# Performance work log

Hardware: AMD Instinct MI355X
Metric: run time of the kernel (lower is better)

## Reference

```python
import jax, jax.numpy as jnp
import numpy as np

N_NODES = 100000
N_EDGES = 1000000
D_IN = 256
D_OUT = 64


def setup_inputs() -> dict:
    key = jax.random.key(0)
    k1, k2, k3, k4, k5, k6 = jax.random.split(key, 6)
    x = jax.random.normal(k1, (N_NODES, D_IN), dtype=jnp.float32)
    # Xavier-style uniform init: stdv = 1/sqrt(output_dim)
    stdv = 1.0 / np.sqrt(D_OUT)
    weight = jax.random.uniform(k2, (D_IN, D_OUT), dtype=jnp.float32, minval=-stdv, maxval=stdv)
    adj_vals = jax.random.uniform(k3, (N_EDGES,), dtype=jnp.float32)
    prelu_a = jnp.full((1,), 0.25, dtype=jnp.float32)  # nn.PReLU default
    row = jax.random.randint(k4, (N_EDGES,), 0, N_NODES, dtype=jnp.int32)
    col = jax.random.randint(k5, (N_EDGES,), 0, N_NODES, dtype=jnp.int32)
    return {"x": x, "weight": weight, "adj_vals": adj_vals, "prelu_a": prelu_a,
            "row": row, "col": col}


def reference(x, weight, adj_vals, prelu_a, row, col):
    # dense GEMM: [N, D_in] @ [D_in, D_out]
    hidden = x @ weight  # gc_drop=0 -> identity dropout
    # sparse adj spmm: out[i] = sum_{e: row[e]=i} adj_vals[e] * hidden[col[e]]
    msg = adj_vals[:, None] * hidden[col]  # [E, D_out]
    agg = jax.ops.segment_sum(msg, row, num_segments=N_NODES)  # [N, D_out]
    # PReLU with single shared slope
    out = jnp.where(agg > 0, agg, prelu_a * agg)
    return out
```

## Files before the change

kernel.cpp:

```cpp
#include <hip/hip_runtime.h>

#define N_NODES 100000
#define N_EDGES 1000000
#define D_IN    256
#define D_OUT   64

#define BKT_SHIFT   4
#define NODES_PER_BKT 16
#define N_BKT       6250
#define BKT_CAP     256
#define EPB         2048
#define BIN_BLOCKS  489
#define GEMM_BLOCKS 782
#define NUM_TILES   6250
#define AGG_BLOCKS  782

typedef __attribute__((ext_vector_type(8))) short short8;
typedef __attribute__((ext_vector_type(4))) float f32x4;
typedef __attribute__((ext_vector_type(4))) unsigned short u16x4;

__device__ __forceinline__ unsigned short f2bf(float f) {
    unsigned int u = __float_as_uint(f);
    u = (u + 0x7fffu + ((u >> 16) & 1u)) >> 16;
    return (unsigned short)u;
}

__device__ __forceinline__ void mfma_store_tile(
    const short8 afrag[8], const unsigned short wT[64][272],
    unsigned short* __restrict__ hiddenBf, int r0, int n16, int quad)
{
    f32x4 acc[4] = {{0.f,0.f,0.f,0.f},{0.f,0.f,0.f,0.f},
                    {0.f,0.f,0.f,0.f},{0.f,0.f,0.f,0.f}};
#pragma unroll
    for (int ct = 0; ct < 4; ++ct) {
#pragma unroll
        for (int kk = 0; kk < 8; ++kk) {
            short8 b = *(const short8*)&wT[ct * 16 + n16][kk * 32 + quad * 8];
            acc[ct] = __builtin_amdgcn_mfma_f32_16x16x32_bf16(
                afrag[kk], b, acc[ct], 0, 0, 0);
        }
    }
#pragma unroll
    for (int ct = 0; ct < 4; ++ct)
#pragma unroll
        for (int reg = 0; reg < 4; ++reg)
            hiddenBf[(size_t)(r0 + quad * 4 + reg) * D_OUT + ct * 16 + n16]
                = f2bf(acc[ct][reg]);
}

__global__ __launch_bounds__(256, 2) void gemm_kernel(
    const float* __restrict__ x, const float* __restrict__ w,
    unsigned short* __restrict__ hiddenBf, int* __restrict__ gCursor)
{
    const int t = threadIdx.x;

    if (blockIdx.x == 0) {
        for (int i = t; i < N_BKT; i += 256) gCursor[i] = 0;
    }

    __shared__ unsigned short wT[64][272];

    for (int i = 0; i < 64; ++i) {
        int idx = t + i * 256;
        int k = idx >> 6, n = idx & 63;
        wT[n][k] = f2bf(w[idx]);
    }
    __syncthreads();

    const int lane = t & 63;
    const int wid  = t >> 6;
    const int n16  = lane & 15;
    const int quad = lane >> 4;

    const int waveGid = blockIdx.x * 4 + wid;
    const int t0 = waveGid * 2;
    if (t0 >= NUM_TILES) return;

    float4 lo[8], hi[8];
    short8 afrag[8];

    {
        const float* xrow = x + (size_t)(t0 * 16 + n16) * D_IN + quad * 8;
#pragma unroll
        for (int kk = 0; kk < 8; ++kk) {
            lo[kk] = *(const float4*)(xrow + kk * 32);
            hi[kk] = *(const float4*)(xrow + kk * 32 + 4);
        }
    }
#pragma unroll
    for (int kk = 0; kk < 8; ++kk) {
        short8 a;
        a[0] = (short)f2bf(lo[kk].x); a[1] = (short)f2bf(lo[kk].y);
        a[2] = (short)f2bf(lo[kk].z); a[3] = (short)f2bf(lo[kk].w);
        a[4] = (short)f2bf(hi[kk].x); a[5] = (short)f2bf(hi[kk].y);
        a[6] = (short)f2bf(hi[kk].z); a[7] = (short)f2bf(hi[kk].w);
        afrag[kk] = a;
    }

    const int t1 = t0 + 1;
    const bool have1 = t1 < NUM_TILES;
    if (have1) {
        const float* xrow = x + (size_t)(t1 * 16 + n16) * D_IN + quad * 8;
#pragma unroll
        for (int kk = 0; kk < 8; ++kk) {
            lo[kk] = *(const float4*)(xrow + kk * 32);
            hi[kk] = *(const float4*)(xrow + kk * 32 + 4);
        }
    }

    mfma_store_tile(afrag, wT, hiddenBf, t0 * 16, n16, quad);

    if (have1) {
#pragma unroll
        for (int kk = 0; kk < 8; ++kk) {
            short8 a;
            a[0] = (short)f2bf(lo[kk].x); a[1] = (short)f2bf(lo[kk].y);
            a[2] = (short)f2bf(lo[kk].z); a[3] = (short)f2bf(lo[kk].w);
            a[4] = (short)f2bf(hi[kk].x); a[5] = (short)f2bf(hi[kk].y);
            a[6] = (short)f2bf(hi[kk].z); a[7] = (short)f2bf(hi[kk].w);
            afrag[kk] = a;
        }
        mfma_store_tile(afrag, wT, hiddenBf, t1 * 16, n16, quad);
    }
}

__global__ __launch_bounds__(256, 2) void bin_kernel(
    const int* __restrict__ row, const int* __restrict__ col,
    const float* __restrict__ adj, int* __restrict__ gCursor,
    int2* __restrict__ edges)
{
    __shared__ int cnt[N_BKT];
    __shared__ int cbase[N_BKT];
    __shared__ int cur[N_BKT];

    const int t  = threadIdx.x;
    const int e0 = blockIdx.x * EPB;

    for (int i = t; i < N_BKT; i += 256) cnt[i] = 0;
    __syncthreads();

    int rreg[8];
#pragma unroll
    for (int u = 0; u < 8; ++u) {
        int e = e0 + t + u * 256;
        rreg[u] = (e < N_EDGES) ? row[e] : -1;
    }
#pragma unroll
    for (int u = 0; u < 8; ++u)
        if (rreg[u] >= 0) atomicAdd(&cnt[rreg[u] >> BKT_SHIFT], 1);
    __syncthreads();

    for (int i = t; i < N_BKT; i += 256) {
        int c = cnt[i];
        cbase[i] = c ? atomicAdd(&gCursor[i], c) : 0;
        cur[i] = 0;
    }
    __syncthreads();

    int cc[8]; float vv[8];
#pragma unroll
    for (int u = 0; u < 8; ++u) {
        int e = e0 + t + u * 256;
        if (rreg[u] >= 0) { cc[u] = col[e]; vv[u] = adj[e]; }
        else              { cc[u] = 0;      vv[u] = 0.f;    }
    }
#pragma unroll
    for (int u = 0; u < 8; ++u) {
        int r = rreg[u];
        if (r >= 0) {
            int b = r >> BKT_SHIFT;
            int off = cbase[b] + atomicAdd(&cur[b], 1);
            if (off < BKT_CAP) {
                unsigned hi = f2bf(vv[u]);
                float hif  = __uint_as_float(hi << 16);
                unsigned lo = f2bf(vv[u] - hif);
                edges[b * BKT_CAP + off] =
                    make_int2(((r & (NODES_PER_BKT - 1)) << 17) | cc[u],
                              (int)((hi << 16) | lo));
            }
        }
    }
}

__global__ __launch_bounds__(512) void agg_mfma_kernel(
    const unsigned short* __restrict__ hiddenBf,
    const int2* __restrict__ edges, const int* __restrict__ gCursor,
    const float* __restrict__ prelu_a, float* __restrict__ out)
{
    __shared__ unsigned short hT[8][64][40];

    const int t    = threadIdx.x;
    const int lane = t & 63;
    const int wid  = t >> 6;
    const int bucket = blockIdx.x * 8 + wid;
    if (bucket >= N_BKT) return;

    const int n16  = lane & 15;
    const int quad = lane >> 4;

    unsigned short (*H)[40] = hT[wid];

    f32x4 acc[4] = {{0.f,0.f,0.f,0.f},{0.f,0.f,0.f,0.f},
                    {0.f,0.f,0.f,0.f},{0.f,0.f,0.f,0.f}};

    const int base = bucket * BKT_CAP;
    int size = gCursor[bucket];
    if (size > BKT_CAP) size = BKT_CAP;

    for (int i0 = 0; i0 < size; i0 += 64) {
        int take = size - i0;
        if (take > 64) take = 64;
        int2 rec = make_int2(0, 0);
        if (lane < take) rec = edges[base + i0 + lane];

#pragma unroll
        for (int s = 0; s < 2; ++s) {
#pragma unroll
            for (int g = 0; g < 2; ++g) {
                int cc[16]; unsigned short hh[16];
#pragma unroll
                for (int u = 0; u < 16; ++u)
                    cc[u] = __builtin_amdgcn_readlane(rec.x, s * 32 + g * 16 + u)
                            & 0x1FFFF;
#pragma unroll
                for (int u = 0; u < 16; ++u)
                    hh[u] = hiddenBf[(size_t)cc[u] * D_OUT + lane];
#pragma unroll
                for (int u = 0; u < 16; u += 4) {
                    u16x4 p;
                    p[0] = hh[u]; p[1] = hh[u + 1];
                    p[2] = hh[u + 2]; p[3] = hh[u + 3];
                    *(u16x4*)&H[lane][g * 16 + u] = p;
                }
            }

            short8 ahi, alo;
#pragma unroll
            for (int j = 0; j < 8; ++j) {
                int e  = s * 32 + quad * 8 + j;
                int rx = __shfl(rec.x, e);
                int ry = __shfl(rec.y, e);
                bool m = (((unsigned)rx >> 17) == (unsigned)n16);
                ahi[j] = m ? (short)((unsigned)ry >> 16) : (short)0;
                alo[j] = m ? (short)(ry & 0xFFFF)        : (short)0;
            }

#pragma unroll
            for (int ct = 0; ct < 4; ++ct) {
                short8 b = *(const short8*)&H[ct * 16 + n16][quad * 8];
                acc[ct] = __builtin_amdgcn_mfma_f32_16x16x32_bf16(
                    ahi, b, acc[ct], 0, 0, 0);
                acc[ct] = __builtin_amdgcn_mfma_f32_16x16x32_bf16(
                    alo, b, acc[ct], 0, 0, 0);
            }
        }
    }

    const float a = prelu_a[0];
    const int node0 = bucket * NODES_PER_BKT;
#pragma unroll
    for (int ct = 0; ct < 4; ++ct)
#pragma unroll
        for (int r = 0; r < 4; ++r) {
            float sv = acc[ct][r];
            out[(size_t)(node0 + quad * 4 + r) * D_OUT + ct * 16 + n16]
                = sv > 0.f ? sv : a * sv;
        }
}

extern "C" void kernel_launch(void* const* d_in, const int* in_sizes, int n_in,
                              void* d_out, int out_size, void* d_ws, size_t ws_size,
                              hipStream_t stream)
{
    const float* x       = (const float*)d_in[0];
    const float* w       = (const float*)d_in[1];
    const float* adj     = (const float*)d_in[2];
    const float* prelu_a = (const float*)d_in[3];
    const int*   row     = (const int*)d_in[4];
    const int*   col     = (const int*)d_in[5];
    float* out = (float*)d_out;

    char* ws = (char*)d_ws;
    unsigned short* hiddenBf = (unsigned short*)(ws);
    int2*  edges    = (int2*)        (ws + 12800000);
    int*   gCursor  = (int*)         (ws + 25600000);

    gemm_kernel<<<GEMM_BLOCKS, 256, 0, stream>>>(x, w, hiddenBf, gCursor);

    bin_kernel<<<BIN_BLOCKS, 256, 0, stream>>>(row, col, adj, gCursor, edges);

    agg_mfma_kernel<<<AGG_BLOCKS, 512, 0, stream>>>(
        hiddenBf, edges, gCursor, prelu_a, out);
}
```

Measured before the change: 240.3 us.

## Fuse edge binning into GEMM kernel using direct global atomics

Measured after the change: 254.8 us. +6.0%, slower.

```diff
diff --git a/kernel.cpp b/kernel.cpp
--- a/kernel.cpp
+++ b/kernel.cpp
@@ -9,10 +9,9 @@
 #define NODES_PER_BKT 16
 #define N_BKT       6250
 #define BKT_CAP     256
-#define EPB         2048
-#define BIN_BLOCKS  489
 #define GEMM_BLOCKS 782
 #define NUM_TILES   6250
+#define EDGES_PER_BLK 1280
 #define AGG_BLOCKS  782
 
 typedef __attribute__((ext_vector_type(8))) short short8;
@@ -48,14 +47,45 @@
                 = f2bf(acc[ct][reg]);
 }
 
-__global__ __launch_bounds__(256, 2) void gemm_kernel(
+__global__ __launch_bounds__(256, 2) void gemm_bin_kernel(
     const float* __restrict__ x, const float* __restrict__ w,
-    unsigned short* __restrict__ hiddenBf, int* __restrict__ gCursor)
+    unsigned short* __restrict__ hiddenBf,
+    const int* __restrict__ row, const int* __restrict__ col,
+    const float* __restrict__ adj, int* __restrict__ gCursor,
+    int2* __restrict__ edges)
 {
     const int t = threadIdx.x;
 
-    if (blockIdx.x == 0) {
-        for (int i = t; i < N_BKT; i += 256) gCursor[i] = 0;
+    {
+        const int e0 = blockIdx.x * EDGES_PER_BLK;
+        int rr[5]; int cc[5]; float vv[5];
+#pragma unroll
+        for (int u = 0; u < 5; ++u) {
+            int e = e0 + u * 256 + t;
+            rr[u] = (e < N_EDGES) ? row[e] : -1;
+        }
+#pragma unroll
+        for (int u = 0; u < 5; ++u) {
+            int e = e0 + u * 256 + t;
+            if (rr[u] >= 0) { cc[u] = col[e]; vv[u] = adj[e]; }
+            else            { cc[u] = 0;      vv[u] = 0.f;    }
+        }
+#pragma unroll
+        for (int u = 0; u < 5; ++u) {
+            int r = rr[u];
+            if (r >= 0) {
+                int b = r >> BKT_SHIFT;
+                int off = atomicAdd(&gCursor[b], 1);
+                if (off < BKT_CAP) {
+                    unsigned hi = f2bf(vv[u]);
+                    float hif   = __uint_as_float(hi << 16);
+                    unsigned lo = f2bf(vv[u] - hif);
+                    edges[b * BKT_CAP + off] =
+                        make_int2(((r & (NODES_PER_BKT - 1)) << 17) | cc[u],
+                                  (int)((hi << 16) | lo));
+                }
+            }
+        }
     }
 
     __shared__ unsigned short wT[64][272];
@@ -124,64 +154,6 @@
     }
 }
 
-__global__ __launch_bounds__(256, 2) void bin_kernel(
-    const int* __restrict__ row, const int* __restrict__ col,
-    const float* __restrict__ adj, int* __restrict__ gCursor,
-    int2* __restrict__ edges)
-{
-    __shared__ int cnt[N_BKT];
-    __shared__ int cbase[N_BKT];
-    __shared__ int cur[N_BKT];
-
-    const int t  = threadIdx.x;
-    const int e0 = blockIdx.x * EPB;
-
-    for (int i = t; i < N_BKT; i += 256) cnt[i] = 0;
-    __syncthreads();
-
-    int rreg[8];
-#pragma unroll
-    for (int u = 0; u < 8; ++u) {
-        int e = e0 + t + u * 256;
-        rreg[u] = (e < N_EDGES) ? row[e] : -1;
-    }
-#pragma unroll
-    for (int u = 0; u < 8; ++u)
-        if (rreg[u] >= 0) atomicAdd(&cnt[rreg[u] >> BKT_SHIFT], 1);
-    __syncthreads();
-
-    for (int i = t; i < N_BKT; i += 256) {
-        int c = cnt[i];
-        cbase[i] = c ? atomicAdd(&gCursor[i], c) : 0;
-        cur[i] = 0;
-    }
-    __syncthreads();
-
-    int cc[8]; float vv[8];
-#pragma unroll
-    for (int u = 0; u < 8; ++u) {
-        int e = e0 + t + u * 256;
-        if (rreg[u] >= 0) { cc[u] = col[e]; vv[u] = adj[e]; }
-        else              { cc[u] = 0;      vv[u] = 0.f;    }
-    }
-#pragma unroll
-    for (int u = 0; u < 8; ++u) {
-        int r = rreg[u];
-        if (r >= 0) {
-            int b = r >> BKT_SHIFT;
-            int off = cbase[b] + atomicAdd(&cur[b], 1);
-            if (off < BKT_CAP) {
-                unsigned hi = f2bf(vv[u]);
-                float hif  = __uint_as_float(hi << 16);
-                unsigned lo = f2bf(vv[u] - hif);
-                edges[b * BKT_CAP + off] =
-                    make_int2(((r & (NODES_PER_BKT - 1)) << 17) | cc[u],
-                              (int)((hi << 16) | lo));
-            }
-        }
-    }
-}
-
 __global__ __launch_bounds__(512) void agg_mfma_kernel(
     const unsigned short* __restrict__ hiddenBf,
     const int2* __restrict__ edges, const int* __restrict__ gCursor,
@@ -285,9 +257,10 @@
     int2*  edges    = (int2*)        (ws + 12800000);
     int*   gCursor  = (int*)         (ws + 25600000);
 
-    gemm_kernel<<<GEMM_BLOCKS, 256, 0, stream>>>(x, w, hiddenBf, gCursor);
-
-    bin_kernel<<<BIN_BLOCKS, 256, 0, stream>>>(row, col, adj, gCursor, edges);
+    hipMemsetAsync(gCursor, 0, N_BKT * sizeof(int), stream);
+
+    gemm_bin_kernel<<<GEMM_BLOCKS, 256, 0, stream>>>(
+        x, w, hiddenBf, row, col, adj, gCursor, edges);
 
     agg_mfma_kernel<<<AGG_BLOCKS, 512, 0, stream>>>(
         hiddenBf, edges, gCursor, prelu_a, out);
```

## Fuse edge binning and GEMM into one launch with shared-memory union

Applied to the files above, without the earlier changes.

Result: faster. 222.1 us (-7.6%).

```diff
diff --git a/kernel.cpp b/kernel.cpp
--- a/kernel.cpp
+++ b/kernel.cpp
@@ -9,8 +9,9 @@
 #define NODES_PER_BKT 16
 #define N_BKT       6250
 #define BKT_CAP     256
-#define EPB         2048
-#define BIN_BLOCKS  489
+
+#define EPB         8192
+#define BIN_BLOCKS  123
 #define GEMM_BLOCKS 782
 #define NUM_TILES   6250
 #define AGG_BLOCKS  782
@@ -48,22 +49,80 @@
                 = f2bf(acc[ct][reg]);
 }
 
-__global__ __launch_bounds__(256, 2) void gemm_kernel(
+__global__ __launch_bounds__(256, 2) void gemm_bin_kernel(
     const float* __restrict__ x, const float* __restrict__ w,
-    unsigned short* __restrict__ hiddenBf, int* __restrict__ gCursor)
-{
+    unsigned short* __restrict__ hiddenBf,
+    const int* __restrict__ row, const int* __restrict__ col,
+    const float* __restrict__ adj, int* __restrict__ gCursor,
+    int2* __restrict__ edges)
+{
+    __shared__ union {
+        struct { int cnt[N_BKT]; int cbase[N_BKT]; } bin;
+        unsigned short wT[64][272];
+    } smem;
+
     const int t = threadIdx.x;
 
-    if (blockIdx.x == 0) {
-        for (int i = t; i < N_BKT; i += 256) gCursor[i] = 0;
-    }
-
-    __shared__ unsigned short wT[64][272];
+    if (blockIdx.x < BIN_BLOCKS) {
+        int* cnt   = smem.bin.cnt;
+        int* cbase = smem.bin.cbase;
+
+        const int e0 = blockIdx.x * EPB;
+
+        for (int i = t; i < N_BKT; i += 256) cnt[i] = 0;
+        __syncthreads();
+
+        int rreg[32];
+#pragma unroll
+        for (int u = 0; u < 32; ++u) {
+            int e = e0 + t + u * 256;
+            rreg[u] = (e < N_EDGES) ? row[e] : -1;
+        }
+#pragma unroll
+        for (int u = 0; u < 32; ++u)
+            if (rreg[u] >= 0) atomicAdd(&cnt[rreg[u] >> BKT_SHIFT], 1);
+        __syncthreads();
+
+        for (int i = t; i < N_BKT; i += 256) {
+            int c = cnt[i];
+            cbase[i] = c ? atomicAdd(&gCursor[i], c) : 0;
+            cnt[i] = 0;
+        }
+        __syncthreads();
+
+#pragma unroll
+        for (int u0 = 0; u0 < 32; u0 += 8) {
+            int cc[8]; float vv[8];
+#pragma unroll
+            for (int u = 0; u < 8; ++u) {
+                int e = e0 + t + (u0 + u) * 256;
+                if (rreg[u0 + u] >= 0) { cc[u] = col[e]; vv[u] = adj[e]; }
+                else                   { cc[u] = 0;      vv[u] = 0.f;    }
+            }
+#pragma unroll
+            for (int u = 0; u < 8; ++u) {
+                int r = rreg[u0 + u];
+                if (r >= 0) {
+                    int b = r >> BKT_SHIFT;
+                    int off = cbase[b] + atomicAdd(&cnt[b], 1);
+                    if (off < BKT_CAP) {
+                        unsigned hi = f2bf(vv[u]);
+                        float hif   = __uint_as_float(hi << 16);
+                        unsigned lo = f2bf(vv[u] - hif);
+                        edges[b * BKT_CAP + off] =
+                            make_int2(((r & (NODES_PER_BKT - 1)) << 17) | cc[u],
+                                      (int)((hi << 16) | lo));
+                    }
+                }
+            }
+        }
+        return;
+    }
 
     for (int i = 0; i < 64; ++i) {
         int idx = t + i * 256;
         int k = idx >> 6, n = idx & 63;
-        wT[n][k] = f2bf(w[idx]);
+        smem.wT[n][k] = f2bf(w[idx]);
     }
     __syncthreads();
 
@@ -72,7 +131,7 @@
     const int n16  = lane & 15;
     const int quad = lane >> 4;
 
-    const int waveGid = blockIdx.x * 4 + wid;
+    const int waveGid = (blockIdx.x - BIN_BLOCKS) * 4 + wid;
     const int t0 = waveGid * 2;
     if (t0 >= NUM_TILES) return;
 
@@ -108,7 +167,7 @@
         }
     }
 
-    mfma_store_tile(afrag, wT, hiddenBf, t0 * 16, n16, quad);
+    mfma_store_tile(afrag, smem.wT, hiddenBf, t0 * 16, n16, quad);
 
     if (have1) {
 #pragma unroll
@@ -120,65 +179,7 @@
             a[6] = (short)f2bf(hi[kk].z); a[7] = (short)f2bf(hi[kk].w);
             afrag[kk] = a;
         }
-        mfma_store_tile(afrag, wT, hiddenBf, t1 * 16, n16, quad);
-    }
-}
-
-__global__ __launch_bounds__(256, 2) void bin_kernel(
-    const int* __restrict__ row, const int* __restrict__ col,
-    const float* __restrict__ adj, int* __restrict__ gCursor,
-    int2* __restrict__ edges)
-{
-    __shared__ int cnt[N_BKT];
-    __shared__ int cbase[N_BKT];
-    __shared__ int cur[N_BKT];
-
-    const int t  = threadIdx.x;
-    const int e0 = blockIdx.x * EPB;
-
-    for (int i = t; i < N_BKT; i += 256) cnt[i] = 0;
-    __syncthreads();
-
-    int rreg[8];
-#pragma unroll
-    for (int u = 0; u < 8; ++u) {
-        int e = e0 + t + u * 256;
-        rreg[u] = (e < N_EDGES) ? row[e] : -1;
-    }
-#pragma unroll
-    for (int u = 0; u < 8; ++u)
-        if (rreg[u] >= 0) atomicAdd(&cnt[rreg[u] >> BKT_SHIFT], 1);
-    __syncthreads();
-
-    for (int i = t; i < N_BKT; i += 256) {
-        int c = cnt[i];
-        cbase[i] = c ? atomicAdd(&gCursor[i], c) : 0;
-        cur[i] = 0;
-    }
-    __syncthreads();
-
-    int cc[8]; float vv[8];
-#pragma unroll
-    for (int u = 0; u < 8; ++u) {
-        int e = e0 + t + u * 256;
-        if (rreg[u] >= 0) { cc[u] = col[e]; vv[u] = adj[e]; }
-        else              { cc[u] = 0;      vv[u] = 0.f;    }
-    }
-#pragma unroll
-    for (int u = 0; u < 8; ++u) {
-        int r = rreg[u];
-        if (r >= 0) {
-            int b = r >> BKT_SHIFT;
-            int off = cbase[b] + atomicAdd(&cur[b], 1);
-            if (off < BKT_CAP) {
-                unsigned hi = f2bf(vv[u]);
-                float hif  = __uint_as_float(hi << 16);
-                unsigned lo = f2bf(vv[u] - hif);
-                edges[b * BKT_CAP + off] =
-                    make_int2(((r & (NODES_PER_BKT - 1)) << 17) | cc[u],
-                              (int)((hi << 16) | lo));
-            }
-        }
+        mfma_store_tile(afrag, smem.wT, hiddenBf, t1 * 16, n16, quad);
     }
 }
 
@@ -285,9 +286,10 @@
     int2*  edges    = (int2*)        (ws + 12800000);
     int*   gCursor  = (int*)         (ws + 25600000);
 
-    gemm_kernel<<<GEMM_BLOCKS, 256, 0, stream>>>(x, w, hiddenBf, gCursor);
-
-    bin_kernel<<<BIN_BLOCKS, 256, 0, stream>>>(row, col, adj, gCursor, edges);
+    hipMemsetAsync(gCursor, 0, N_BKT * sizeof(int), stream);
+
+    gemm_bin_kernel<<<BIN_BLOCKS + GEMM_BLOCKS, 256, 0, stream>>>(
+        x, w, hiddenBf, row, col, adj, gCursor, edges);
 
     agg_mfma_kernel<<<AGG_BLOCKS, 512, 0, stream>>>(
         hiddenBf, edges, gCursor, prelu_a, out);
```
